# Kernel optimization log

Hardware: AMD Instinct MI355X
Metric: run time of the kernel (lower is better)

The kernel has to match this reference:

```python
import jax, jax.numpy as jnp
import numpy as np


def setup_inputs() -> dict:
    key = jax.random.key(0)
    k1, k2, k3, k4, k5 = jax.random.split(key, 5)
    dim, hidden = 64, 128
    x = jax.random.normal(k1, (32, 128, 128, dim), dtype=jnp.float32)
    # torch Linear stores (out,in); we store transposed so y = x @ W + b
    W_expand = jax.random.normal(k2, (dim, hidden), dtype=jnp.float32) * (1.0 / np.sqrt(dim))
    b_expand = jax.random.normal(k3, (hidden,), dtype=jnp.float32) * 0.01
    W_restore = jax.random.normal(k4, (hidden, 1), dtype=jnp.float32) * (1.0 / np.sqrt(hidden))
    b_restore = jax.random.normal(k5, (1,), dtype=jnp.float32) * 0.01
    return {
        "x": x,
        "W_expand": W_expand,
        "b_expand": b_expand,
        "W_restore": W_restore,
        "b_restore": b_restore,
        "kernel_size": 2,
        "stride": 2,
    }


def reference(x, W_expand, b_expand, W_restore, b_restore, kernel_size, stride):
    b, r, c, d = x.shape
    sr = (r - kernel_size) // stride + 1
    sc = (c - kernel_size) // stride + 1
    s = stride  # original code slices stride x stride windows
    # gather all windows at once: (b, sr, s, sc, s, d)
    ri = (jnp.arange(sr) * stride)[:, None] + jnp.arange(s)[None, :]
    ci = (jnp.arange(sc) * stride)[:, None] + jnp.arange(s)[None, :]
    win = x[:, ri[:, :, None, None], ci[None, None, :, :], :]
    # -> (b, sr, sc, s*s, d)
    win = win.transpose(0, 1, 3, 2, 4, 5).reshape(b, sr, sc, s * s, d)
    # tiny MLP attention weights per window element
    h = jnp.tanh(jnp.einsum('bqpwd,dh->bqpwh', win, W_expand) + b_expand)
    logit = jax.nn.sigmoid(jnp.einsum('bqpwh,ho->bqpwo', h, W_restore)[..., 0] + b_restore[0])
    w = jax.nn.softmax(logit, axis=-1)  # over window elements
    out = jnp.sum(win * w[..., None], axis=3)  # (b, sr, sc, d)
    return out
```

## Files before the change

### kernel.cpp

```cpp
#include <hip/hip_runtime.h>


typedef __attribute__((ext_vector_type(8))) short short8;
typedef __attribute__((ext_vector_type(4))) float floatx4;

#define B_   32
#define R_   128
#define C_   128
#define D_   64
#define H_   128
#define NW_  (B_ * 64 * 64)
#define NGRP_ (NW_ / 4)
#define NBLK_ (NGRP_ / 4)

#define L2E_  1.4426950408889634f
#define T2L_  2.8853900817779268f

__device__ __forceinline__ unsigned short f2bf_rne(float f) {
  union { float f; unsigned int u; } v; v.f = f;
  unsigned int u = v.u;
  u += 0x7fffu + ((u >> 16) & 1u);
  return (unsigned short)(u >> 16);
}

__device__ __forceinline__ unsigned int pk_bf16(float lo, float hi) {
  unsigned int a = __builtin_bit_cast(unsigned int, lo) + 0x8000u;
  unsigned int b = __builtin_bit_cast(unsigned int, hi) + 0x8000u;
  return __builtin_amdgcn_perm(b, a, 0x07060302u);
}

template <int CTRL>
__device__ __forceinline__ float dpp_add(float x) {
  int xi = __builtin_bit_cast(int, x);
  int yi = __builtin_amdgcn_update_dpp(0, xi, CTRL, 0xf, 0xf, true);
  return x + __builtin_bit_cast(float, yi);
}
#define DPP_XOR1   0xB1
#define DPP_XOR3   0x1B
#define DPP_XOR7   0x141
#define DPP_XOR15  0x140
__device__ __forceinline__ float row_reduce16(float x) {
  x = dpp_add<DPP_XOR1>(x);
  x = dpp_add<DPP_XOR3>(x);
  x = dpp_add<DPP_XOR7>(x);
  x = dpp_add<DPP_XOR15>(x);
  return x;
}

__global__ void prep_kernel(const float* __restrict__ We,
                            unsigned short* __restrict__ F)
{
  int t = blockIdx.x * 256 + threadIdx.x;
  int j    = t & 7;
  int lane = (t >> 3) & 63;
  int fi   = t >> 9;
  int n  = fi >> 1, ks = fi & 1;
  int quad = lane >> 4, c = lane & 15;
  F[t] = f2bf_rne(We[(ks * 32 + quad * 8 + j) * 128 + n * 16 + c]);
}

__global__ __launch_bounds__(256, 2) void softpool_kernel(
    const float* __restrict__ x, const unsigned short* __restrict__ F,
    const float* __restrict__ be, const float* __restrict__ Wr,
    const float* __restrict__ br, float* __restrict__ out)
{
  const int lane = threadIdx.x & 63;
  const int wv   = threadIdx.x >> 6;
  const int c    = lane & 15;
  const int quad = lane >> 4;

  const int g = blockIdx.x * 4 + wv;

  short8 Bf[8][2];
#pragma unroll
  for (int n = 0; n < 8; ++n)
#pragma unroll
    for (int ks = 0; ks < 2; ++ks)
      Bf[n][ks] = *(const short8*)&F[((n * 2 + ks) * 64 + lane) * 8];

  const int w0   = g * 4 + (c >> 2);
  const int elem = c & 3;
  const int bb = w0 >> 12;
  const int qq = (w0 >> 6) & 63;
  const int pp = w0 & 63;
  const float* xp = x + (((bb * R_ + (qq * 2 + (elem >> 1))) * C_
                          + (pp * 2 + (elem & 1))) * D_) + quad * 8;
  floatx4 a0 = *(const floatx4*)(xp);
  floatx4 a1 = *(const floatx4*)(xp + 4);
  floatx4 a2 = *(const floatx4*)(xp + 32);
  floatx4 a3 = *(const floatx4*)(xp + 36);

  const int wq = g * 4 + quad;
  const int b2 = wq >> 12;
  const int q2 = (wq >> 6) & 63;
  const int p2i = wq & 63;
  const float* xw = x + (((b2 * R_ + q2 * 2) * C_ + p2i * 2) * D_) + c * 4;
  floatx4 x0 = *(const floatx4*)(xw);
  floatx4 x1 = *(const floatx4*)(xw + D_);
  floatx4 x2 = *(const floatx4*)(xw + C_ * D_);
  floatx4 x3 = *(const floatx4*)(xw + C_ * D_ + D_);

  float beK[8], wr2[8], swr = 0.f;
#pragma unroll
  for (int n = 0; n < 8; ++n) {
    float w = Wr[n * 16 + c];
    beK[n] = be[n * 16 + c] * T2L_;
    wr2[n] = -2.0f * w;
    swr += w;
  }
  const float brN = -L2E_ * br[0];

  union { unsigned int u[4]; short8 v; } A0u, A1u;
  A0u.u[0] = pk_bf16(a0[0], a0[1]); A0u.u[1] = pk_bf16(a0[2], a0[3]);
  A0u.u[2] = pk_bf16(a1[0], a1[1]); A0u.u[3] = pk_bf16(a1[2], a1[3]);
  A1u.u[0] = pk_bf16(a2[0], a2[1]); A1u.u[1] = pk_bf16(a2[2], a2[3]);
  A1u.u[2] = pk_bf16(a3[0], a3[1]); A1u.u[3] = pk_bf16(a3[2], a3[3]);

  floatx4 acc[8];
#pragma unroll
  for (int n = 0; n < 8; ++n) {
    floatx4 z = {0.f, 0.f, 0.f, 0.f};
    z = __builtin_amdgcn_mfma_f32_16x16x32_bf16(A0u.v, Bf[n][0], z, 0, 0, 0);
    acc[n] = __builtin_amdgcn_mfma_f32_16x16x32_bf16(A1u.v, Bf[n][1], z, 0, 0, 0);
  }

  float p0 = swr, p1 = swr, p2 = swr, p3 = swr;
#pragma unroll
  for (int n = 0; n < 8; ++n) {
    float e0 = __builtin_amdgcn_exp2f(fmaf(acc[n][0], T2L_, beK[n]));
    float e1 = __builtin_amdgcn_exp2f(fmaf(acc[n][1], T2L_, beK[n]));
    float e2 = __builtin_amdgcn_exp2f(fmaf(acc[n][2], T2L_, beK[n]));
    float e3 = __builtin_amdgcn_exp2f(fmaf(acc[n][3], T2L_, beK[n]));
    p0 = fmaf(wr2[n], __builtin_amdgcn_rcpf(e0 + 1.0f), p0);
    p1 = fmaf(wr2[n], __builtin_amdgcn_rcpf(e1 + 1.0f), p1);
    p2 = fmaf(wr2[n], __builtin_amdgcn_rcpf(e2 + 1.0f), p2);
    p3 = fmaf(wr2[n], __builtin_amdgcn_rcpf(e3 + 1.0f), p3);
  }
  p0 = row_reduce16(p0);
  p1 = row_reduce16(p1);
  p2 = row_reduce16(p2);
  p3 = row_reduce16(p3);
  float l0 = __builtin_amdgcn_rcpf(1.0f + __builtin_amdgcn_exp2f(fmaf(p0, -L2E_, brN)));
  float l1 = __builtin_amdgcn_rcpf(1.0f + __builtin_amdgcn_exp2f(fmaf(p1, -L2E_, brN)));
  float l2 = __builtin_amdgcn_rcpf(1.0f + __builtin_amdgcn_exp2f(fmaf(p2, -L2E_, brN)));
  float l3 = __builtin_amdgcn_rcpf(1.0f + __builtin_amdgcn_exp2f(fmaf(p3, -L2E_, brN)));
  float s0 = __builtin_amdgcn_exp2f(l0 * L2E_);
  float s1 = __builtin_amdgcn_exp2f(l1 * L2E_);
  float s2 = __builtin_amdgcn_exp2f(l2 * L2E_);
  float s3 = __builtin_amdgcn_exp2f(l3 * L2E_);
  float inv = __builtin_amdgcn_rcpf(s0 + s1 + s2 + s3);
  float w0f = s0 * inv, w1f = s1 * inv, w2f = s2 * inv, w3f = s3 * inv;

  floatx4 o = x0 * w0f + x1 * w1f + x2 * w2f + x3 * w3f;
  *(floatx4*)(out + (long)wq * 64 + c * 4) = o;
}

extern "C" void kernel_launch(void* const* d_in, const int* in_sizes, int n_in,
                              void* d_out, int out_size, void* d_ws, size_t ws_size,
                              hipStream_t stream) {
  const float* x  = (const float*)d_in[0];
  const float* We = (const float*)d_in[1];
  const float* be = (const float*)d_in[2];
  const float* Wr = (const float*)d_in[3];
  const float* br = (const float*)d_in[4];
  float* out = (float*)d_out;
  unsigned short* F = (unsigned short*)d_ws;

  prep_kernel<<<32, 256, 0, stream>>>(We, F);
  softpool_kernel<<<NBLK_, 256, 0, stream>>>(x, F, be, Wr, br, out);
}
```

Before: 217.4 us.

## Make softpool kernel persistent with software-prefetched next-group loads

The grid shrinks from one block per 16 windows to a fixed 1024 blocks, and each wave now loops over several window groups with a fixed stride through x. Inside the loop the loads for the next iteration are issued before the MFMA and activation math for the current one, so memory latency overlaps compute. The B-fragment and bias setup is amortised across iterations. In exchange the kernel holds a double set of input registers, which may lower occupancy, and has fewer waves in flight overall.

```diff
diff --git a/kernel.cpp b/kernel.cpp
--- a/kernel.cpp
+++ b/kernel.cpp
@@ -11,7 +11,12 @@
 #define H_   128
 #define NW_  (B_ * 64 * 64)
 #define NGRP_ (NW_ / 4)
-#define NBLK_ (NGRP_ / 4)
+#define NBLK_ 1024
+#define NWAVE_ (NBLK_ * 4)
+#define L_   (NGRP_ / NWAVE_)
+
+#define XSTEP_ (4L * R_ * C_ * D_)
+#define OSTEP_ ((long)NWAVE_ * 4 * 64)
 
 #define L2E_  1.4426950408889634f
 #define T2L_  2.8853900817779268f
@@ -69,36 +74,12 @@
   const int c    = lane & 15;
   const int quad = lane >> 4;
 
-  const int g = blockIdx.x * 4 + wv;
-
   short8 Bf[8][2];
 #pragma unroll
   for (int n = 0; n < 8; ++n)
 #pragma unroll
     for (int ks = 0; ks < 2; ++ks)
       Bf[n][ks] = *(const short8*)&F[((n * 2 + ks) * 64 + lane) * 8];
-
-  const int w0   = g * 4 + (c >> 2);
-  const int elem = c & 3;
-  const int bb = w0 >> 12;
-  const int qq = (w0 >> 6) & 63;
-  const int pp = w0 & 63;
-  const float* xp = x + (((bb * R_ + (qq * 2 + (elem >> 1))) * C_
-                          + (pp * 2 + (elem & 1))) * D_) + quad * 8;
-  floatx4 a0 = *(const floatx4*)(xp);
-  floatx4 a1 = *(const floatx4*)(xp + 4);
-  floatx4 a2 = *(const floatx4*)(xp + 32);
-  floatx4 a3 = *(const floatx4*)(xp + 36);
-
-  const int wq = g * 4 + quad;
-  const int b2 = wq >> 12;
-  const int q2 = (wq >> 6) & 63;
-  const int p2i = wq & 63;
-  const float* xw = x + (((b2 * R_ + q2 * 2) * C_ + p2i * 2) * D_) + c * 4;
-  floatx4 x0 = *(const floatx4*)(xw);
-  floatx4 x1 = *(const floatx4*)(xw + D_);
-  floatx4 x2 = *(const floatx4*)(xw + C_ * D_);
-  floatx4 x3 = *(const floatx4*)(xw + C_ * D_ + D_);
 
   float beK[8], wr2[8], swr = 0.f;
 #pragma unroll
@@ -110,49 +91,93 @@
   }
   const float brN = -L2E_ * br[0];
 
-  union { unsigned int u[4]; short8 v; } A0u, A1u;
-  A0u.u[0] = pk_bf16(a0[0], a0[1]); A0u.u[1] = pk_bf16(a0[2], a0[3]);
-  A0u.u[2] = pk_bf16(a1[0], a1[1]); A0u.u[3] = pk_bf16(a1[2], a1[3]);
-  A1u.u[0] = pk_bf16(a2[0], a2[1]); A1u.u[1] = pk_bf16(a2[2], a2[3]);
-  A1u.u[2] = pk_bf16(a3[0], a3[1]); A1u.u[3] = pk_bf16(a3[2], a3[3]);
+  const int gw = blockIdx.x * 4 + wv;
 
-  floatx4 acc[8];
+  const int w0   = gw * 4 + (c >> 2);
+  const int elem = c & 3;
+  const int bb = w0 >> 12;
+  const int qq = (w0 >> 6) & 63;
+  const int pp = w0 & 63;
+  const float* xp = x + (((bb * R_ + (qq * 2 + (elem >> 1))) * C_
+                          + (pp * 2 + (elem & 1))) * D_) + quad * 8;
+
+  const int wq0 = gw * 4 + quad;
+  const int b2 = wq0 >> 12;
+  const int q2 = (wq0 >> 6) & 63;
+  const int p2i = wq0 & 63;
+  const float* xw = x + (((b2 * R_ + q2 * 2) * C_ + p2i * 2) * D_) + c * 4;
+  float* op = out + (long)wq0 * 64 + c * 4;
+
+  floatx4 a0 = *(const floatx4*)(xp);
+  floatx4 a1 = *(const floatx4*)(xp + 4);
+  floatx4 a2 = *(const floatx4*)(xp + 32);
+  floatx4 a3 = *(const floatx4*)(xp + 36);
+  floatx4 x0 = *(const floatx4*)(xw);
+  floatx4 x1 = *(const floatx4*)(xw + D_);
+  floatx4 x2 = *(const floatx4*)(xw + C_ * D_);
+  floatx4 x3 = *(const floatx4*)(xw + C_ * D_ + D_);
+
+  for (int it = 0; it < L_; ++it) {
+    const long nd = (it < L_ - 1) ? XSTEP_ : 0;
+    const float* xpn = xp + nd;
+    const float* xwn = xw + nd;
+    floatx4 na0 = *(const floatx4*)(xpn);
+    floatx4 na1 = *(const floatx4*)(xpn + 4);
+    floatx4 na2 = *(const floatx4*)(xpn + 32);
+    floatx4 na3 = *(const floatx4*)(xpn + 36);
+    floatx4 nx0 = *(const floatx4*)(xwn);
+    floatx4 nx1 = *(const floatx4*)(xwn + D_);
+    floatx4 nx2 = *(const floatx4*)(xwn + C_ * D_);
+    floatx4 nx3 = *(const floatx4*)(xwn + C_ * D_ + D_);
+
+    union { unsigned int u[4]; short8 v; } A0u, A1u;
+    A0u.u[0] = pk_bf16(a0[0], a0[1]); A0u.u[1] = pk_bf16(a0[2], a0[3]);
+    A0u.u[2] = pk_bf16(a1[0], a1[1]); A0u.u[3] = pk_bf16(a1[2], a1[3]);
+    A1u.u[0] = pk_bf16(a2[0], a2[1]); A1u.u[1] = pk_bf16(a2[2], a2[3]);
+    A1u.u[2] = pk_bf16(a3[0], a3[1]); A1u.u[3] = pk_bf16(a3[2], a3[3]);
+
+    floatx4 acc[8];
 #pragma unroll
-  for (int n = 0; n < 8; ++n) {
-    floatx4 z = {0.f, 0.f, 0.f, 0.f};
-    z = __builtin_amdgcn_mfma_f32_16x16x32_bf16(A0u.v, Bf[n][0], z, 0, 0, 0);
-    acc[n] = __builtin_amdgcn_mfma_f32_16x16x32_bf16(A1u.v, Bf[n][1], z, 0, 0, 0);
+    for (int n = 0; n < 8; ++n) {
+      floatx4 z = {0.f, 0.f, 0.f, 0.f};
+      z = __builtin_amdgcn_mfma_f32_16x16x32_bf16(A0u.v, Bf[n][0], z, 0, 0, 0);
+      acc[n] = __builtin_amdgcn_mfma_f32_16x16x32_bf16(A1u.v, Bf[n][1], z, 0, 0, 0);
+    }
+
+    float p0 = swr, p1 = swr, p2 = swr, p3 = swr;
+#pragma unroll
+    for (int n = 0; n < 8; ++n) {
+      float e0 = __builtin_amdgcn_exp2f(fmaf(acc[n][0], T2L_, beK[n]));
+      float e1 = __builtin_amdgcn_exp2f(fmaf(acc[n][1], T2L_, beK[n]));
+      float e2 = __builtin_amdgcn_exp2f(fmaf(acc[n][2], T2L_, beK[n]));
+      float e3 = __builtin_amdgcn_exp2f(fmaf(acc[n][3], T2L_, beK[n]));
+      p0 = fmaf(wr2[n], __builtin_amdgcn_rcpf(e0 + 1.0f), p0);
+      p1 = fmaf(wr2[n], __builtin_amdgcn_rcpf(e1 + 1.0f), p1);
+      p2 = fmaf(wr2[n], __builtin_amdgcn_rcpf(e2 + 1.0f), p2);
+      p3 = fmaf(wr2[n], __builtin_amdgcn_rcpf(e3 + 1.0f), p3);
+    }
+    p0 = row_reduce16(p0);
+    p1 = row_reduce16(p1);
+    p2 = row_reduce16(p2);
+    p3 = row_reduce16(p3);
+    float l0 = __builtin_amdgcn_rcpf(1.0f + __builtin_amdgcn_exp2f(fmaf(p0, -L2E_, brN)));
+    float l1 = __builtin_amdgcn_rcpf(1.0f + __builtin_amdgcn_exp2f(fmaf(p1, -L2E_, brN)));
+    float l2 = __builtin_amdgcn_rcpf(1.0f + __builtin_amdgcn_exp2f(fmaf(p2, -L2E_, brN)));
+    float l3 = __builtin_amdgcn_rcpf(1.0f + __builtin_amdgcn_exp2f(fmaf(p3, -L2E_, brN)));
+    float s0 = __builtin_amdgcn_exp2f(l0 * L2E_);
+    float s1 = __builtin_amdgcn_exp2f(l1 * L2E_);
+    float s2 = __builtin_amdgcn_exp2f(l2 * L2E_);
+    float s3 = __builtin_amdgcn_exp2f(l3 * L2E_);
+    float inv = __builtin_amdgcn_rcpf(s0 + s1 + s2 + s3);
+    float w0f = s0 * inv, w1f = s1 * inv, w2f = s2 * inv, w3f = s3 * inv;
+
+    floatx4 o = x0 * w0f + x1 * w1f + x2 * w2f + x3 * w3f;
+    *(floatx4*)(op) = o;
+
+    xp = xpn; xw = xwn; op += OSTEP_;
+    a0 = na0; a1 = na1; a2 = na2; a3 = na3;
+    x0 = nx0; x1 = nx1; x2 = nx2; x3 = nx3;
   }
-
-  float p0 = swr, p1 = swr, p2 = swr, p3 = swr;
-#pragma unroll
-  for (int n = 0; n < 8; ++n) {
-    float e0 = __builtin_amdgcn_exp2f(fmaf(acc[n][0], T2L_, beK[n]));
-    float e1 = __builtin_amdgcn_exp2f(fmaf(acc[n][1], T2L_, beK[n]));
-    float e2 = __builtin_amdgcn_exp2f(fmaf(acc[n][2], T2L_, beK[n]));
-    float e3 = __builtin_amdgcn_exp2f(fmaf(acc[n][3], T2L_, beK[n]));
-    p0 = fmaf(wr2[n], __builtin_amdgcn_rcpf(e0 + 1.0f), p0);
-    p1 = fmaf(wr2[n], __builtin_amdgcn_rcpf(e1 + 1.0f), p1);
-    p2 = fmaf(wr2[n], __builtin_amdgcn_rcpf(e2 + 1.0f), p2);
-    p3 = fmaf(wr2[n], __builtin_amdgcn_rcpf(e3 + 1.0f), p3);
-  }
-  p0 = row_reduce16(p0);
-  p1 = row_reduce16(p1);
-  p2 = row_reduce16(p2);
-  p3 = row_reduce16(p3);
-  float l0 = __builtin_amdgcn_rcpf(1.0f + __builtin_amdgcn_exp2f(fmaf(p0, -L2E_, brN)));
-  float l1 = __builtin_amdgcn_rcpf(1.0f + __builtin_amdgcn_exp2f(fmaf(p1, -L2E_, brN)));
-  float l2 = __builtin_amdgcn_rcpf(1.0f + __builtin_amdgcn_exp2f(fmaf(p2, -L2E_, brN)));
-  float l3 = __builtin_amdgcn_rcpf(1.0f + __builtin_amdgcn_exp2f(fmaf(p3, -L2E_, brN)));
-  float s0 = __builtin_amdgcn_exp2f(l0 * L2E_);
-  float s1 = __builtin_amdgcn_exp2f(l1 * L2E_);
-  float s2 = __builtin_amdgcn_exp2f(l2 * L2E_);
-  float s3 = __builtin_amdgcn_exp2f(l3 * L2E_);
-  float inv = __builtin_amdgcn_rcpf(s0 + s1 + s2 + s3);
-  float w0f = s0 * inv, w1f = s1 * inv, w2f = s2 * inv, w3f = s3 * inv;
-
-  floatx4 o = x0 * w0f + x1 * w1f + x2 * w2f + x3 * w3f;
-  *(floatx4*)(out + (long)wq * 64 + c * 4) = o;
 }
 
 extern "C" void kernel_launch(void* const* d_in, const int* in_sizes, int n_in,
```

Measured after the change: 210.0 us. 1.04x faster.
